# Optimization experiments

Hardware: AMD Instinct MI355X
Metric: run time of the kernel (lower is better)

Reference implementation:

```python
import jax, jax.numpy as jnp
import numpy as np

N = 100000
E = 1600000
CARDS = [1000, 100, 50, 10000]
EDIMS = [10, 6, 5, 18]  # emb_dim_from_card = clip(round(1.8*card**0.25), 4, 24)
NUM_IN = 32
HID = 128
EPS = 1e-5


def setup_inputs() -> dict:
    key = jax.random.key(0)
    ks = jax.random.split(key, 24)
    x_num = jax.random.normal(ks[0], (N, NUM_IN), dtype=jnp.float32)
    cols = [jax.random.randint(jax.random.fold_in(ks[1], j), (N,), 0, c) for j, c in enumerate(CARDS)]
    x_cat = jnp.stack(cols, axis=1)
    edge_index = jax.random.randint(ks[2], (2, E), 0, N)
    embs = {f"emb{j}": 0.02 * jax.random.normal(ks[3 + j], (c, d), dtype=jnp.float32)
            for j, (c, d) in enumerate(zip(CARDS, EDIMS))}
    in_dim = NUM_IN + sum(EDIMS)  # 71
    def lin(k, fi, fo):
        s = 1.0 / np.sqrt(fi)
        return jax.random.uniform(k, (fi, fo), jnp.float32, -s, s)
    params = dict(
        w_in=lin(ks[7], in_dim, HID), b_in=jnp.zeros((HID,), jnp.float32),
        w1l=lin(ks[8], HID, HID), b1l=jnp.zeros((HID,), jnp.float32), w1r=lin(ks[9], HID, HID),
        w2l=lin(ks[10], HID, HID), b2l=jnp.zeros((HID,), jnp.float32), w2r=lin(ks[11], HID, HID),
        g1=jnp.ones((HID,), jnp.float32), be1=jnp.zeros((HID,), jnp.float32),
        g2=jnp.ones((HID,), jnp.float32), be2=jnp.zeros((HID,), jnp.float32),
        wh1=lin(ks[12], HID, 64), bh1=jnp.zeros((64,), jnp.float32),
        wh2=lin(ks[13], 64, 1), bh2=jnp.zeros((1,), jnp.float32),
    )
    return {"x_num": x_num, "x_cat": x_cat, "edge_index": edge_index, **embs, **params}


def _layer_norm(x, g, b):
    mu = jnp.mean(x, axis=-1, keepdims=True)
    var = jnp.var(x, axis=-1, keepdims=True)
    return (x - mu) * jax.lax.rsqrt(var + EPS) * g + b


def _sage_conv(x, src, dst, wl, bl, wr):
    # PyG SAGEConv(mean): lin_l(mean_{j in N(i)} x_j) + lin_r(x_i)
    agg = jax.ops.segment_sum(x[src], dst, num_segments=N)
    cnt = jax.ops.segment_sum(jnp.ones((src.shape[0],), x.dtype), dst, num_segments=N)
    mean = agg / jnp.maximum(cnt, 1.0)[:, None]
    return mean @ wl + bl + x @ wr


def reference(x_num, x_cat, edge_index,
              emb0, emb1, emb2, emb3,
              w_in, b_in, w1l, b1l, w1r, w2l, b2l, w2r,
              g1, be1, g2, be2, wh1, bh1, wh2, bh2):
    # eval mode: dropout is identity
    zc = jnp.concatenate([emb0[x_cat[:, 0]], emb1[x_cat[:, 1]],
                          emb2[x_cat[:, 2]], emb3[x_cat[:, 3]]], axis=1)
    x = jnp.concatenate([x_num, zc], axis=1)
    x = jax.nn.relu(x @ w_in + b_in)
    src, dst = edge_index[0], edge_index[1]
    x1 = jax.nn.relu(_layer_norm(_sage_conv(x, src, dst, w1l, b1l, w1r), g1, be1))
    x = x + 0.5 * x1
    x2 = jax.nn.relu(_layer_norm(_sage_conv(x, src, dst, w2l, b2l, w2r), g2, be2))
    x = x + 0.5 * x2
    h = jax.nn.relu(x @ wh1 + bh1)
    return (h @ wh2 + bh2)[:, 0]
```

## Files before the change

### kernel.cpp

```cpp
#include <hip/hip_runtime.h>

#define HID 128

typedef __attribute__((ext_vector_type(8))) short short8;
typedef __attribute__((ext_vector_type(4))) float f32x4;

__device__ __forceinline__ float bf2f(unsigned short u) {
    unsigned int x = ((unsigned int)u) << 16;
    return __builtin_bit_cast(float, x);
}
__device__ __forceinline__ unsigned short f2bf(float f) {
    unsigned int u = __builtin_bit_cast(unsigned int, f);
    u += 0x7fffu + ((u >> 16) & 1u);
    return (unsigned short)(u >> 16);
}

__global__ __launch_bounds__(256) void k_prepw(const float* __restrict__ s1, int k1,
    const float* __restrict__ s2, int k2, int Kp, int N,
    unsigned short* __restrict__ whi, unsigned short* __restrict__ wlo)
{
    int i = blockIdx.x * 256 + threadIdx.x;
    if (i >= Kp * N) return;
    int k = i / N, nn = i - k * N;
    float v = 0.f;
    if (k < k1) v = s1[(size_t)k * N + nn];
    else if (k < k1 + k2) v = s2[(size_t)(k - k1) * N + nn];
    unsigned short h = f2bf(v);
    unsigned short l = f2bf(v - bf2f(h));
    size_t o = ((size_t)(k >> 5) * N + nn) * 32 + (k & 31);
    whi[o] = h; wlo[o] = l;
}

__global__ __launch_bounds__(256) void k_stack0(
    const float* __restrict__ xnum, const int* __restrict__ xcat,
    const float* __restrict__ e0, const float* __restrict__ e1,
    const float* __restrict__ e2, const float* __restrict__ e3,
    unsigned short* __restrict__ A0, int n)
{
    int g = blockIdx.x * 256 + threadIdx.x;
    int r = g / 6, c = g - r * 6;
    if (r >= n) return;
    int4 cc = ((const int4*)xcat)[r];
    float v[16];
    int base = c * 16;
    #pragma unroll
    for (int j = 0; j < 16; ++j) {
        int col = base + j;
        float val;
        if      (col < 32) val = xnum[(size_t)r * 32 + col];
        else if (col < 42) val = e0[(size_t)cc.x * 10 + (col - 32)];
        else if (col < 48) val = e1[(size_t)cc.y * 6  + (col - 42)];
        else if (col < 53) val = e2[(size_t)cc.z * 5  + (col - 48)];
        else if (col < 71) val = e3[(size_t)cc.w * 18 + (col - 53)];
        else               val = 0.f;
        v[j] = val;
    }
    unsigned int ph[8];
    #pragma unroll
    for (int j = 0; j < 8; ++j)
        ph[j] = (unsigned int)f2bf(v[2*j]) | ((unsigned int)f2bf(v[2*j+1]) << 16);
    unsigned int* dh = (unsigned int*)(A0 + (size_t)r * 96 + base);
    uint4 a; a.x = ph[0]; a.y = ph[1]; a.z = ph[2]; a.w = ph[3];
    uint4 b; b.x = ph[4]; b.y = ph[5]; b.z = ph[6]; b.w = ph[7];
    ((uint4*)dh)[0] = a; ((uint4*)dh)[1] = b;
}

__global__ __launch_bounds__(256) void k_part(const int* __restrict__ esrc,
    const int* __restrict__ edst, int* __restrict__ gCur, int2* __restrict__ ebuf,
    int ecount, int chunk, int cap)
{
    __shared__ int hist[512];
    __shared__ int base[512];
    int t = threadIdx.x;
    hist[t] = 0; hist[t + 256] = 0;
    __syncthreads();
    int start = blockIdx.x * chunk;
    int end = start + chunk < ecount ? start + chunk : ecount;
    for (int i = start + t; i < end; i += 256)
        atomicAdd(&hist[edst[i] >> 8], 1);
    __syncthreads();
    for (int bk = t; bk < 512; bk += 256) {
        int h = hist[bk];
        base[bk] = h ? atomicAdd(&gCur[bk], h) : 0;
        hist[bk] = 0;
    }
    __syncthreads();
    for (int i = start + t; i < end; i += 256) {
        int d = edst[i];
        int b = d >> 8;
        int slot = atomicAdd(&hist[b], 1);
        int pos = base[b] + slot;
        if (pos < cap)
            ebuf[(size_t)b * cap + pos] = make_int2(esrc[i], d);
    }
}

__global__ __launch_bounds__(512) void k_scanb(const int* __restrict__ gCur,
    int* __restrict__ bBase, int* __restrict__ row_ptr, int nbuck, int n, int ecount)
{
    __shared__ int sm[512];
    int t = threadIdx.x;
    int c = (t < nbuck) ? gCur[t] : 0;
    sm[t] = c;
    __syncthreads();
    for (int d = 1; d < 512; d <<= 1) {
        int v = (t >= d) ? sm[t - d] : 0;
        __syncthreads();
        sm[t] += v;
        __syncthreads();
    }
    if (t < nbuck) bBase[t] = sm[t] - c;
    if (t == 0) row_ptr[n] = ecount;
}

__global__ __launch_bounds__(256) void k_bcsr(const int2* __restrict__ ebuf,
    const int* __restrict__ gCur, const int* __restrict__ bBase,
    int* __restrict__ row_ptr, int* __restrict__ col, int cap, int n)
{
    __shared__ int h[256];
    __shared__ int sm[256];
    int b = blockIdx.x, t = threadIdx.x;
    int cnt = gCur[b];
    int nb0 = b << 8;
    const int2* eb = ebuf + (size_t)b * cap;
    h[t] = 0;
    __syncthreads();
    for (int i = t; i < cnt; i += 256)
        atomicAdd(&h[eb[i].y & 255], 1);
    __syncthreads();
    int hv = h[t];
    sm[t] = hv;
    __syncthreads();
    for (int d = 1; d < 256; d <<= 1) {
        int v = (t >= d) ? sm[t - d] : 0;
        __syncthreads();
        sm[t] += v;
        __syncthreads();
    }
    int excl = sm[t] - hv;
    int gb = bBase[b];
    int g = nb0 + t;
    if (g < n) row_ptr[g] = gb + excl;
    __syncthreads();
    h[t] = excl;
    __syncthreads();
    for (int i = t; i < cnt; i += 256) {
        int2 e = eb[i];
        int slot = atomicAdd(&h[e.y & 255], 1);
        col[gb + slot] = e.x;
    }
}

__global__ __launch_bounds__(256) void k_agg(
    const unsigned short* __restrict__ xh, unsigned short* __restrict__ mh, int SK,
    const int* __restrict__ row_ptr, const int* __restrict__ col, int n,
    int zr, int emax)
{
    int lane = threadIdx.x & 63;
    int qw  = lane >> 4;
    int l16 = lane & 15;
    int node = blockIdx.x * 4 + (threadIdx.x >> 6);
    if (node >= n) return;
    node = __builtin_amdgcn_readfirstlane(node);
    int s = row_ptr[node], e = row_ptr[node + 1];
    int deg = e - s;
    float a0 = 0.f, a1 = 0.f, a2 = 0.f, a3 = 0.f;
    float a4 = 0.f, a5 = 0.f, a6 = 0.f, a7 = 0.f;
    size_t cOff = (size_t)l16 * 8;

    auto accum = [&](uint4 r) {
        a0 += __builtin_bit_cast(float, r.x << 16);
        a1 += __builtin_bit_cast(float, r.x & 0xffff0000u);
        a2 += __builtin_bit_cast(float, r.y << 16);
        a3 += __builtin_bit_cast(float, r.y & 0xffff0000u);
        a4 += __builtin_bit_cast(float, r.z << 16);
        a5 += __builtin_bit_cast(float, r.z & 0xffff0000u);
        a6 += __builtin_bit_cast(float, r.w << 16);
        a7 += __builtin_bit_cast(float, r.w & 0xffff0000u);
    };

    int em1 = emax - 1;
    for (int p = s + qw; p < e; p += 16) {
        int p1 = p + 4, p2 = p + 8, p3 = p + 12;
        int q1 = p1 < em1 ? p1 : em1;
        int q2 = p2 < em1 ? p2 : em1;
        int q3 = p3 < em1 ? p3 : em1;
        int t0 = col[p];
        int t1 = col[q1];
        int t2 = col[q2];
        int t3 = col[q3];
        int c0 = t0;
        int c1 = (p1 < e) ? t1 : zr;
        int c2 = (p2 < e) ? t2 : zr;
        int c3 = (p3 < e) ? t3 : zr;
        uint4 r0 = *(const uint4*)(xh + (size_t)c0 * SK + cOff);
        uint4 r1 = *(const uint4*)(xh + (size_t)c1 * SK + cOff);
        uint4 r2 = *(const uint4*)(xh + (size_t)c2 * SK + cOff);
        uint4 r3 = *(const uint4*)(xh + (size_t)c3 * SK + cOff);
        accum(r0); accum(r1); accum(r2); accum(r3);
    }

    a0 += __shfl_xor(a0, 16); a0 += __shfl_xor(a0, 32);
    a1 += __shfl_xor(a1, 16); a1 += __shfl_xor(a1, 32);
    a2 += __shfl_xor(a2, 16); a2 += __shfl_xor(a2, 32);
    a3 += __shfl_xor(a3, 16); a3 += __shfl_xor(a3, 32);
    a4 += __shfl_xor(a4, 16); a4 += __shfl_xor(a4, 32);
    a5 += __shfl_xor(a5, 16); a5 += __shfl_xor(a5, 32);
    a6 += __shfl_xor(a6, 16); a6 += __shfl_xor(a6, 32);
    a7 += __shfl_xor(a7, 16); a7 += __shfl_xor(a7, 32);

    if (qw == 0) {
        float inv = 1.f / (float)(deg > 1 ? deg : 1);
        uint4 o;
        o.x = (unsigned int)f2bf(a0 * inv) | ((unsigned int)f2bf(a1 * inv) << 16);
        o.y = (unsigned int)f2bf(a2 * inv) | ((unsigned int)f2bf(a3 * inv) << 16);
        o.z = (unsigned int)f2bf(a4 * inv) | ((unsigned int)f2bf(a5 * inv) << 16);
        o.w = (unsigned int)f2bf(a6 * inv) | ((unsigned int)f2bf(a7 * inv) << 16);
        *(uint4*)(mh + (size_t)node * SK + cOff) = o;
    }
}

template<int NC, int KT8, int EPI>
__global__ __launch_bounds__(256) void k_gemm(
    const unsigned short* __restrict__ A, int SK,
    const unsigned short* __restrict__ Whi, const unsigned short* __restrict__ Wlo,
    const float* __restrict__ bias,
    const float* __restrict__ g, const float* __restrict__ be,
    const unsigned short* __restrict__ Src, int SSK,
    unsigned short* __restrict__ Dst, int DSK,
    const float* __restrict__ wh2, const float* __restrict__ bh2, float* __restrict__ outp,
    int n)
{
    constexpr int NT = NC / 64;
    __shared__ float Cb[32][NC + 4];
    int t = threadIdx.x;
    int lane = t & 63, w = t >> 6;
    int l15 = lane & 15, kg = lane >> 4;
    int m0 = blockIdx.x * 64;

    size_t aoff[4];
    #pragma unroll
    for (int mt = 0; mt < 4; ++mt) {
        int r = m0 + mt * 16 + l15;
        r = r < n ? r : n - 1;
        aoff[mt] = (size_t)r * SK + kg * 8;
    }
    size_t nb[NT];
    #pragma unroll
    for (int nt = 0; nt < NT; ++nt)
        nb[nt] = (size_t)(w * (NC / 4) + nt * 16 + l15) * 32 + kg * 8;

    f32x4 acc[4][NT];
    #pragma unroll
    for (int mt = 0; mt < 4; ++mt)
        #pragma unroll
        for (int nt = 0; nt < NT; ++nt)
            acc[mt][nt] = (f32x4)(0.f);

    short8 ah[4], bh[NT], bl[NT];
    #pragma unroll
    for (int mt = 0; mt < 4; ++mt)
        ah[mt] = *(const short8*)(A + aoff[mt]);
    #pragma unroll
    for (int nt = 0; nt < NT; ++nt) {
        bh[nt] = *(const short8*)(Whi + nb[nt]);
        bl[nt] = *(const short8*)(Wlo + nb[nt]);
    }

    #pragma unroll 1
    for (int s = 0; s < KT8; ++s) {
        int s2 = (s + 1 < KT8) ? s + 1 : s;
        int koff2 = s2 * 32;
        short8 ah2[4], bh2[NT], bl2[NT];
        #pragma unroll
        for (int mt = 0; mt < 4; ++mt)
            ah2[mt] = *(const short8*)(A + aoff[mt] + koff2);
        #pragma unroll
        for (int nt = 0; nt < NT; ++nt) {
            bh2[nt] = *(const short8*)(Whi + (size_t)s2 * NC * 32 + nb[nt]);
            bl2[nt] = *(const short8*)(Wlo + (size_t)s2 * NC * 32 + nb[nt]);
        }
        #pragma unroll
        for (int mt = 0; mt < 4; ++mt)
            #pragma unroll
            for (int nt = 0; nt < NT; ++nt)
                acc[mt][nt] = __builtin_amdgcn_mfma_f32_16x16x32_bf16(ah[mt], bh[nt], acc[mt][nt], 0, 0, 0);
        #pragma unroll
        for (int mt = 0; mt < 4; ++mt)
            #pragma unroll
            for (int nt = 0; nt < NT; ++nt)
                acc[mt][nt] = __builtin_amdgcn_mfma_f32_16x16x32_bf16(ah[mt], bl[nt], acc[mt][nt], 0, 0, 0);
        #pragma unroll
        for (int mt = 0; mt < 4; ++mt) ah[mt] = ah2[mt];
        #pragma unroll
        for (int nt = 0; nt < NT; ++nt) { bh[nt] = bh2[nt]; bl[nt] = bl2[nt]; }
    }

    constexpr int CW = NC / 8;
    int er = t >> 3, q = t & 7;
    int cb = q * CW;

    #pragma unroll
    for (int p = 0; p < 2; ++p) {
        if (p) __syncthreads();
        #pragma unroll
        for (int mt2 = 0; mt2 < 2; ++mt2) {
            int mt = 2 * p + mt2;
            #pragma unroll
            for (int nt = 0; nt < NT; ++nt)
                #pragma unroll
                for (int r = 0; r < 4; ++r)
                    Cb[mt2 * 16 + kg * 4 + r][w * (NC / 4) + nt * 16 + l15] = acc[mt][nt][r];
        }
        __syncthreads();

        int gr = m0 + p * 32 + er;

        if (EPI == 0) {
            if (gr < n) {
                #pragma unroll
                for (int i = 0; i < CW / 4; ++i) {
                    int c = cb + 4 * i;
                    float4 v  = *(const float4*)&Cb[er][c];
                    float4 bi = *(const float4*)&bias[c];
                    ushort4 hv = make_ushort4(f2bf(fmaxf(v.x + bi.x, 0.f)),
                                              f2bf(fmaxf(v.y + bi.y, 0.f)),
                                              f2bf(fmaxf(v.z + bi.z, 0.f)),
                                              f2bf(fmaxf(v.w + bi.w, 0.f)));
                    *(ushort4*)(Dst + (size_t)gr * DSK + c) = hv;
                }
            }
        } else if (EPI == 1) {
            float s = 0.f, ss = 0.f;
            #pragma unroll
            for (int i = 0; i < CW / 4; ++i) {
                int c = cb + 4 * i;
                float4 v  = *(const float4*)&Cb[er][c];
                float4 bi = *(const float4*)&bias[c];
                float a0 = v.x + bi.x, a1 = v.y + bi.y, a2 = v.z + bi.z, a3 = v.w + bi.w;
                s  += a0 + a1 + a2 + a3;
                ss += a0 * a0 + a1 * a1 + a2 * a2 + a3 * a3;
            }
            s  += __shfl_xor(s, 1);  s  += __shfl_xor(s, 2);  s  += __shfl_xor(s, 4);
            ss += __shfl_xor(ss, 1); ss += __shfl_xor(ss, 2); ss += __shfl_xor(ss, 4);
            float mu  = s * (1.f / NC);
            float var = ss * (1.f / NC) - mu * mu;
            float rs  = rsqrtf(var + 1e-5f);
            if (gr < n) {
                #pragma unroll
                for (int i = 0; i < CW / 4; ++i) {
                    int c = cb + 4 * i;
                    float4 v  = *(const float4*)&Cb[er][c];
                    float4 bi = *(const float4*)&bias[c];
                    float4 gg = *(const float4*)&g[c];
                    float4 bb = *(const float4*)&be[c];
                    float r0 = fmaxf((v.x + bi.x - mu) * rs * gg.x + bb.x, 0.f);
                    float r1 = fmaxf((v.y + bi.y - mu) * rs * gg.y + bb.y, 0.f);
                    float r2 = fmaxf((v.z + bi.z - mu) * rs * gg.z + bb.z, 0.f);
                    float r3 = fmaxf((v.w + bi.w - mu) * rs * gg.w + bb.w, 0.f);
                    ushort4 rh = *(const ushort4*)(Src + (size_t)gr * SSK + c);
                    ushort4 hv = make_ushort4(f2bf(bf2f(rh.x) + 0.5f * r0),
                                              f2bf(bf2f(rh.y) + 0.5f * r1),
                                              f2bf(bf2f(rh.z) + 0.5f * r2),
                                              f2bf(bf2f(rh.w) + 0.5f * r3));
                    *(ushort4*)(Dst + (size_t)gr * DSK + c) = hv;
                }
            }
        } else {
            float s = 0.f;
            #pragma unroll
            for (int i = 0; i < CW / 4; ++i) {
                int c = cb + 4 * i;
                float4 v  = *(const float4*)&Cb[er][c];
                float4 bi = *(const float4*)&bias[c];
                float4 w2 = *(const float4*)&wh2[c];
                s += fmaxf(v.x + bi.x, 0.f) * w2.x + fmaxf(v.y + bi.y, 0.f) * w2.y
                   + fmaxf(v.z + bi.z, 0.f) * w2.z + fmaxf(v.w + bi.w, 0.f) * w2.w;
            }
            s += __shfl_xor(s, 1); s += __shfl_xor(s, 2); s += __shfl_xor(s, 4);
            if (q == 0 && gr < n) outp[gr] = s + bh2[0];
        }
    }
}

extern "C" void kernel_launch(void* const* d_in, const int* in_sizes, int n_in,
                              void* d_out, int out_size, void* d_ws, size_t ws_size,
                              hipStream_t stream)
{
    const float* xnum = (const float*)d_in[0];
    const int*   xcat = (const int*)d_in[1];
    const int*   eidx = (const int*)d_in[2];
    const float* e0   = (const float*)d_in[3];
    const float* e1   = (const float*)d_in[4];
    const float* e2   = (const float*)d_in[5];
    const float* e3   = (const float*)d_in[6];
    const float* w_in = (const float*)d_in[7];
    const float* b_in = (const float*)d_in[8];
    const float* w1l  = (const float*)d_in[9];
    const float* b1l  = (const float*)d_in[10];
    const float* w1r  = (const float*)d_in[11];
    const float* w2l  = (const float*)d_in[12];
    const float* b2l  = (const float*)d_in[13];
    const float* w2r  = (const float*)d_in[14];
    const float* g1   = (const float*)d_in[15];
    const float* be1  = (const float*)d_in[16];
    const float* g2   = (const float*)d_in[17];
    const float* be2  = (const float*)d_in[18];
    const float* wh1  = (const float*)d_in[19];
    const float* bh1  = (const float*)d_in[20];
    const float* wh2  = (const float*)d_in[21];
    const float* bh2  = (const float*)d_in[22];

    int n = in_sizes[0] / 32;
    int ecount = in_sizes[2] / 2;
    const int* esrc = eidx;
    const int* edst = eidx + ecount;

    char* ws = (char*)d_ws;
    size_t off = 0;
    auto alloc = [&](size_t bytes) -> void* {
        void* p = ws + off;
        off += (bytes + 255) & ~(size_t)255;
        return p;
    };
    unsigned short* A1 = (unsigned short*)alloc((size_t)(n + 1) * 256 * 2);
    unsigned short* A3 = A1;
    unsigned short* A2 = (unsigned short*)alloc((size_t)(n + 1) * 256 * 2);
    unsigned short* A0 = A2;
    unsigned short* w0h = (unsigned short*)alloc((size_t)96 * 128 * 2);
    unsigned short* w0l = (unsigned short*)alloc((size_t)96 * 128 * 2);
    unsigned short* w1h = (unsigned short*)alloc((size_t)256 * 128 * 2);
    unsigned short* w1lo= (unsigned short*)alloc((size_t)256 * 128 * 2);
    unsigned short* w2h = (unsigned short*)alloc((size_t)256 * 128 * 2);
    unsigned short* w2lo= (unsigned short*)alloc((size_t)256 * 128 * 2);
    unsigned short* whh = (unsigned short*)alloc((size_t)128 * 64 * 2);
    unsigned short* whl = (unsigned short*)alloc((size_t)128 * 64 * 2);
    int nbuck = (n + 255) >> 8;
    int cap = ecount / nbuck + ecount / (2 * nbuck) + 256;
    int* gCur    = (int*)alloc(512 * 4);
    int* bBase   = (int*)alloc(512 * 4);
    int* row_ptr = (int*)alloc((size_t)(n + 1) * 4);
    int* col     = (int*)alloc((size_t)ecount * 4);
    int2* ebuf   = (int2*)alloc((size_t)nbuck * cap * 8);
    (void)ws_size; (void)n_in; (void)out_size;

    int gemmBlocks = (n + 63) / 64;
    int aggBlocks = (n + 3) / 4;

    k_prepw<<<(96 * 128 + 255) / 256, 256, 0, stream>>>(w_in, 71, nullptr, 0, 96, 128, w0h, w0l);
    k_prepw<<<(256 * 128 + 255) / 256, 256, 0, stream>>>(w1l, 128, w1r, 128, 256, 128, w1h, w1lo);
    k_prepw<<<(256 * 128 + 255) / 256, 256, 0, stream>>>(w2l, 128, w2r, 128, 256, 128, w2h, w2lo);
    k_prepw<<<(128 * 64 + 255) / 256, 256, 0, stream>>>(wh1, 128, nullptr, 0, 128, 64, whh, whl);

    hipMemsetAsync(A1 + (size_t)n * 256, 0, 256 * 2, stream);
    hipMemsetAsync(A2 + (size_t)n * 256, 0, 256 * 2, stream);
    k_stack0<<<((size_t)n * 6 + 255) / 256, 256, 0, stream>>>(xnum, xcat, e0, e1, e2, e3, A0, n);

    hipMemsetAsync(gCur, 0, 512 * 4, stream);
    int nblkP = 512;
    int chunk = (ecount + nblkP - 1) / nblkP;
    k_part<<<nblkP, 256, 0, stream>>>(esrc, edst, gCur, ebuf, ecount, chunk, cap);
    k_scanb<<<1, 512, 0, stream>>>(gCur, bBase, row_ptr, nbuck, n, ecount);
    k_bcsr<<<nbuck, 256, 0, stream>>>(ebuf, gCur, bBase, row_ptr, col, cap, n);

    k_gemm<128, 3, 0><<<gemmBlocks, 256, 0, stream>>>(
        A0, 96, w0h, w0l, b_in,
        nullptr, nullptr, nullptr, 0,
        A1 + 128, 256,
        nullptr, nullptr, nullptr, n);

    k_agg<<<aggBlocks, 256, 0, stream>>>(A1 + 128, A1, 256, row_ptr, col, n, n, ecount);
    k_gemm<128, 8, 1><<<gemmBlocks, 256, 0, stream>>>(
        A1, 256, w1h, w1lo, b1l,
        g1, be1, A1 + 128, 256,
        A2 + 128, 256,
        nullptr, nullptr, nullptr, n);

    k_agg<<<aggBlocks, 256, 0, stream>>>(A2 + 128, A2, 256, row_ptr, col, n, n, ecount);
    k_gemm<128, 8, 1><<<gemmBlocks, 256, 0, stream>>>(
        A2, 256, w2h, w2lo, b2l,
        g2, be2, A2 + 128, 256,
        A3, 128,
        nullptr, nullptr, nullptr, n);

    k_gemm<64, 4, 2><<<gemmBlocks, 256, 0, stream>>>(
        A3, 128, whh, whl, bh1,
        nullptr, nullptr, nullptr, 0,
        nullptr, 0,
        wh2, bh2, (float*)d_out, n);
}
```

Before: 458.8 us.

## Merge weight prep and memsets into one kernel; drop GEMM register prefetch

Replaces four weight-split launches and three memset calls with a single kernel that branches on block index, which cuts launch overhead between small setup steps. Separately, the GEMM main loop stops double-buffering its A/B fragments in registers and loads them at the start of each iteration. This lowers register pressure and may raise occupancy, but load latency is no longer hidden behind the previous step's MFMAs.

```diff
diff --git a/kernel.cpp b/kernel.cpp
--- a/kernel.cpp
+++ b/kernel.cpp
@@ -15,20 +15,43 @@
     return (unsigned short)(u >> 16);
 }
 
-__global__ __launch_bounds__(256) void k_prepw(const float* __restrict__ s1, int k1,
-    const float* __restrict__ s2, int k2, int Kp, int N,
+__device__ __forceinline__ void prep_one(const float* __restrict__ s1, int k1,
+    const float* __restrict__ s2, int N, int i,
     unsigned short* __restrict__ whi, unsigned short* __restrict__ wlo)
 {
-    int i = blockIdx.x * 256 + threadIdx.x;
-    if (i >= Kp * N) return;
     int k = i / N, nn = i - k * N;
-    float v = 0.f;
-    if (k < k1) v = s1[(size_t)k * N + nn];
-    else if (k < k1 + k2) v = s2[(size_t)(k - k1) * N + nn];
+    float v = (k < k1) ? s1[(size_t)k * N + nn]
+                       : (s2 ? s2[(size_t)(k - k1) * N + nn] : 0.f);
     unsigned short h = f2bf(v);
     unsigned short l = f2bf(v - bf2f(h));
     size_t o = ((size_t)(k >> 5) * N + nn) * 32 + (k & 31);
     whi[o] = h; wlo[o] = l;
+}
+
+__global__ __launch_bounds__(256) void k_prep(
+    const float* __restrict__ w_in, const float* __restrict__ w1l,
+    const float* __restrict__ w1r, const float* __restrict__ w2l,
+    const float* __restrict__ w2r, const float* __restrict__ wh1,
+    unsigned short* __restrict__ w0h, unsigned short* __restrict__ w0l,
+    unsigned short* __restrict__ w1h, unsigned short* __restrict__ w1lo,
+    unsigned short* __restrict__ w2h, unsigned short* __restrict__ w2lo,
+    unsigned short* __restrict__ whh, unsigned short* __restrict__ whl,
+    unsigned short* __restrict__ z1, unsigned short* __restrict__ z2,
+    int* __restrict__ gCur)
+{
+    int b = blockIdx.x, t = threadIdx.x;
+    if (b < 48) {
+        prep_one(w_in, 71, nullptr, 128, b * 256 + t, w0h, w0l);
+    } else if (b < 176) {
+        prep_one(w1l, 128, w1r, 128, (b - 48) * 256 + t, w1h, w1lo);
+    } else if (b < 304) {
+        prep_one(w2l, 128, w2r, 128, (b - 176) * 256 + t, w2h, w2lo);
+    } else if (b < 336) {
+        prep_one(wh1, 128, nullptr, 64, (b - 304) * 256 + t, whh, whl);
+    } else {
+        z1[t] = 0; z2[t] = 0;
+        gCur[t] = 0; gCur[t + 256] = 0;
+    }
 }
 
 __global__ __launch_bounds__(256) void k_stack0(
@@ -257,28 +280,18 @@
         for (int nt = 0; nt < NT; ++nt)
             acc[mt][nt] = (f32x4)(0.f);
 
-    short8 ah[4], bh[NT], bl[NT];
-    #pragma unroll
-    for (int mt = 0; mt < 4; ++mt)
-        ah[mt] = *(const short8*)(A + aoff[mt]);
-    #pragma unroll
-    for (int nt = 0; nt < NT; ++nt) {
-        bh[nt] = *(const short8*)(Whi + nb[nt]);
-        bl[nt] = *(const short8*)(Wlo + nb[nt]);
-    }
-
     #pragma unroll 1
     for (int s = 0; s < KT8; ++s) {
-        int s2 = (s + 1 < KT8) ? s + 1 : s;
-        int koff2 = s2 * 32;
-        short8 ah2[4], bh2[NT], bl2[NT];
+        int koff = s * 32;
+        short8 ah[4];
         #pragma unroll
         for (int mt = 0; mt < 4; ++mt)
-            ah2[mt] = *(const short8*)(A + aoff[mt] + koff2);
+            ah[mt] = *(const short8*)(A + aoff[mt] + koff);
+        short8 bh[NT], bl[NT];
         #pragma unroll
         for (int nt = 0; nt < NT; ++nt) {
-            bh2[nt] = *(const short8*)(Whi + (size_t)s2 * NC * 32 + nb[nt]);
-            bl2[nt] = *(const short8*)(Wlo + (size_t)s2 * NC * 32 + nb[nt]);
+            bh[nt] = *(const short8*)(Whi + (size_t)s * NC * 32 + nb[nt]);
+            bl[nt] = *(const short8*)(Wlo + (size_t)s * NC * 32 + nb[nt]);
         }
         #pragma unroll
         for (int mt = 0; mt < 4; ++mt)
@@ -290,10 +303,6 @@
             #pragma unroll
             for (int nt = 0; nt < NT; ++nt)
                 acc[mt][nt] = __builtin_amdgcn_mfma_f32_16x16x32_bf16(ah[mt], bl[nt], acc[mt][nt], 0, 0, 0);
-        #pragma unroll
-        for (int mt = 0; mt < 4; ++mt) ah[mt] = ah2[mt];
-        #pragma unroll
-        for (int nt = 0; nt < NT; ++nt) { bh[nt] = bh2[nt]; bl[nt] = bl2[nt]; }
     }
 
     constexpr int CW = NC / 8;
@@ -447,16 +456,13 @@
     int gemmBlocks = (n + 63) / 64;
     int aggBlocks = (n + 3) / 4;
 
-    k_prepw<<<(96 * 128 + 255) / 256, 256, 0, stream>>>(w_in, 71, nullptr, 0, 96, 128, w0h, w0l);
-    k_prepw<<<(256 * 128 + 255) / 256, 256, 0, stream>>>(w1l, 128, w1r, 128, 256, 128, w1h, w1lo);
-    k_prepw<<<(256 * 128 + 255) / 256, 256, 0, stream>>>(w2l, 128, w2r, 128, 256, 128, w2h, w2lo);
-    k_prepw<<<(128 * 64 + 255) / 256, 256, 0, stream>>>(wh1, 128, nullptr, 0, 128, 64, whh, whl);
-
-    hipMemsetAsync(A1 + (size_t)n * 256, 0, 256 * 2, stream);
-    hipMemsetAsync(A2 + (size_t)n * 256, 0, 256 * 2, stream);
+    k_prep<<<337, 256, 0, stream>>>(
+        w_in, w1l, w1r, w2l, w2r, wh1,
+        w0h, w0l, w1h, w1lo, w2h, w2lo, whh, whl,
+        A1 + (size_t)n * 256, A2 + (size_t)n * 256, gCur);
+
     k_stack0<<<((size_t)n * 6 + 255) / 256, 256, 0, stream>>>(xnum, xcat, e0, e1, e2, e3, A0, n);
 
-    hipMemsetAsync(gCur, 0, 512 * 4, stream);
     int nblkP = 512;
     int chunk = (ecount + nblkP - 1) / nblkP;
     k_part<<<nblkP, 256, 0, stream>>>(esrc, edst, gCur, ebuf, ecount, chunk, cap);
```

New measurement: 434.3 us (median of 2 runs). 1.06x faster.
